# Performance work log

Measured on AMD Instinct MI355X. Metric: run time of the kernel, lower is better.

The kernel has to match this reference:

```python
import jax, jax.numpy as jnp
import numpy as np

ALPHA = 100.0  # self.softmax_alpha


def _interp_nearest(x, size):
    # torch F.interpolate mode='nearest': src_idx = floor(dst_idx * H_in / H_out)
    H, W = x.shape[-2], x.shape[-1]
    h, w = size
    ri = (jnp.arange(h) * H) // h
    ci = (jnp.arange(w) * W) // w
    return x[:, :, ri, :][:, :, :, ci]


def _interp_bilinear_ac(x, size):
    # torch F.interpolate mode='bilinear', align_corners=True
    H, W = x.shape[-2], x.shape[-1]
    h, w = size

    def coords(n_out, n_in):
        if n_out == 1:
            return jnp.zeros((1,), jnp.float32)
        return jnp.arange(n_out, dtype=jnp.float32) * ((n_in - 1) / (n_out - 1))

    ry, rx = coords(h, H), coords(w, W)
    y0 = jnp.floor(ry).astype(jnp.int32)
    x0 = jnp.floor(rx).astype(jnp.int32)
    y1 = jnp.clip(y0 + 1, 0, H - 1)
    x1 = jnp.clip(x0 + 1, 0, W - 1)
    wy = (ry - y0.astype(jnp.float32))[None, None, :, None]
    wx = (rx - x0.astype(jnp.float32))[None, None, None, :]
    rows = x[:, :, y0, :] * (1.0 - wy) + x[:, :, y1, :] * wy  # (n,c,h,W)
    return rows[:, :, :, x0] * (1.0 - wx) + rows[:, :, :, x1] * wx  # (n,c,h,w)


def _warp(unalign_fb, fa, fa_parse, fb, fb_parse, alpha):
    n, c, h, w = fa.shape
    c2 = unalign_fb.shape[1]
    hw = h * w
    # center and channel-normalize features per spatial location
    fa = fa - jnp.mean(fa, axis=(2, 3), keepdims=True)
    fb = fb - jnp.mean(fb, axis=(2, 3), keepdims=True)
    fa = fa.reshape(n, c, hw)
    fb = fb.reshape(n, c, hw)
    fa = fa / jnp.linalg.norm(fa, axis=1, keepdims=True)
    fb = fb / jnp.linalg.norm(fb, axis=1, keepdims=True)
    ufb = unalign_fb.reshape(n, c2, hw)
    mask_a = (fa_parse.reshape(n, -1, hw)[:, 1:, :] != 0).astype(fa.dtype)  # (n,K,hw)
    mask_b = (fb_parse.reshape(n, -1, hw)[:, 1:, :] != 0).astype(fb.dtype)
    local_fa = fa[:, None, :, :] * mask_a[:, :, None, :]  # (n,K,c,hw)
    local_fb = fb[:, None, :, :] * mask_b[:, :, None, :]  # (n,K,c,hw)
    # energy[n,k,q,p] = sum_c local_fb[n,k,c,q] * local_fa[n,k,c,p]
    energy = jnp.einsum('nkcq,nkcp->nkqp', local_fb, local_fa) * alpha
    corr = jax.nn.softmax(energy, axis=2)  # softmax over fb locations q
    warped = jnp.einsum('ncq,nkqp->nkcp', ufb, corr)  # (n,K,c2,hw)
    combined = (warped * mask_a[:, :, None, :]).sum(axis=1)  # (n,c2,hw)
    norm = jnp.maximum(mask_a.sum(axis=1, keepdims=True), 1.0)  # (n,1,hw)
    aligned = combined / norm
    return aligned.reshape(n, c2, h, w)


def setup_inputs() -> dict:
    key = jax.random.key(0)
    k1, k2, k3, k4, k5 = jax.random.split(key, 5)
    return {
        'unalign_fb': jax.random.normal(k1, (1, 64, 256, 256), jnp.float32),
        'fa': jax.random.normal(k2, (1, 256, 64, 64), jnp.float32),
        'fa_parse': jax.random.randint(k3, (1, 4, 256, 256), 0, 2).astype(jnp.int32),
        'fb': jax.random.normal(k4, (1, 256, 64, 64), jnp.float32),
        'fb_parse': jax.random.randint(k5, (1, 4, 256, 256), 0, 2).astype(jnp.int32),
    }


def reference(unalign_fb, fa, fa_parse, fb, fb_parse):
    raw_hw = unalign_fb.shape[-2:]
    feat_hw = fa.shape[-2:]
    fa_p = _interp_nearest(fa_parse, feat_hw)
    fb_p = _interp_nearest(fb_parse, feat_hw)
    ufb = _interp_bilinear_ac(unalign_fb, fb.shape[-2:])
    aligned = _warp(ufb, fa, fa_p, fb, fb_p, ALPHA)
    return _interp_bilinear_ac(aligned, raw_hw)
```

## Files before the change

### kernel.cpp

```cpp
#include <hip/hip_runtime.h>
#include <math.h>

#define HW 4096
#define CC 256
#define C2 64
#define E50f 1.928749848e-22f

typedef unsigned short USH;
typedef __attribute__((ext_vector_type(8))) _Float16 f16x8;
typedef __attribute__((ext_vector_type(8))) short bf8;
typedef __attribute__((ext_vector_type(4))) float f32x4;

__device__ __forceinline__ USH f2bf(float x) {
    unsigned u = __float_as_uint(x);
    u += 0x7fff + ((u >> 16) & 1);
    return (USH)(u >> 16);
}
__device__ __forceinline__ USH f2h(float x) {
    _Float16 h = (_Float16)x;
    return *(USH*)&h;
}

__device__ __forceinline__ void gl2lds16(const USH* g, USH* l) {
    __builtin_amdgcn_global_load_lds(
        (const __attribute__((address_space(1))) void*)g,
        (__attribute__((address_space(3))) void*)l, 16, 0, 0);
}

__global__ void k_prep1(const float* __restrict__ fa, const float* __restrict__ fb,
                        float* __restrict__ mu,
                        const float* __restrict__ ufb_src, const int* __restrict__ fb_parse,
                        USH* __restrict__ vtT, float* __restrict__ bgp) {
    __shared__ float4 sred[256];
    int t = threadIdx.x;
    if (blockIdx.x < 512) {
        int b = blockIdx.x;
        const float* src = (b < CC) ? (fa + b * HW) : (fb + (b - CC) * HW);
        float s = 0.f;
        for (int q = t; q < HW; q += 256) s += src[q];
        sred[t].x = s;
        __syncthreads();
        for (int st = 128; st > 0; st >>= 1) {
            if (t < st) sred[t].x += sred[t + st].x;
            __syncthreads();
        }
        if (t == 0) mu[b] = sred[0].x * (1.0f / HW);
        return;
    }
    int bid = blockIdx.x - 512;
    int pblk = bid & 15, c = bid >> 4;
    int p = pblk * 256 + t;
    int j = p >> 6, i = p & 63;
    int off = (4 * j) * 256 + 4 * i;
    float m0 = (fb_parse[1 * 65536 + off] != 0) ? 1.f : 0.f;
    float m1 = (fb_parse[2 * 65536 + off] != 0) ? 1.f : 0.f;
    float m2 = (fb_parse[3 * 65536 + off] != 0) ? 1.f : 0.f;
    float ry = j * (255.0f / 63.0f);
    int y0 = (int)ry; y0 = min(y0, 255); int y1 = min(y0 + 1, 255);
    float wy = ry - (float)y0;
    float rx = i * (255.0f / 63.0f);
    int x0 = (int)rx; x0 = min(x0, 255); int x1 = min(x0 + 1, 255);
    float wx = rx - (float)x0;
    const float* sc = ufb_src + c * 65536;
    float r0 = sc[y0 * 256 + x0] * (1.f - wx) + sc[y0 * 256 + x1] * wx;
    float r1 = sc[y1 * 256 + x0] * (1.f - wx) + sc[y1 * 256 + x1] * wx;
    float v = r0 * (1.f - wy) + r1 * wy;
    size_t cbase = (size_t)(p >> 5) * 8192 + (p & 31);
    vtT[cbase + (0 * 65 + c) * 32] = f2bf(v * m0);
    vtT[cbase + (1 * 65 + c) * 32] = f2bf(v * m1);
    vtT[cbase + (2 * 65 + c) * 32] = f2bf(v * m2);
    if (c == 0) {
        vtT[cbase + 64 * 32]  = f2bf(m0);
        vtT[cbase + 129 * 32] = f2bf(m1);
        vtT[cbase + 194 * 32] = f2bf(m2);
        for (int m = 195; m < 256; ++m) vtT[cbase + m * 32] = 0;
    }
    sred[t] = make_float4(v, v * m0, v * m1, v * m2);
    __syncthreads();
    for (int st = 128; st > 0; st >>= 1) {
        if (t < st) {
            float4 o = sred[t + st];
            sred[t].x += o.x; sred[t].y += o.y; sred[t].z += o.z; sred[t].w += o.w;
        }
        __syncthreads();
    }
    if (t == 0) {
        float4 r = sred[0];
        bgp[pblk * 320 + 256 + c]     = r.x;
        bgp[pblk * 320 + 0 * 65 + c]  = r.y;
        bgp[pblk * 320 + 1 * 65 + c]  = r.z;
        bgp[pblk * 320 + 2 * 65 + c]  = r.w;
    }
    __syncthreads();
    if (c == 0) {
        sred[t] = make_float4(m0, m1, m2, 0.f);
        __syncthreads();
        for (int st = 128; st > 0; st >>= 1) {
            if (t < st) {
                float4 o = sred[t + st];
                sred[t].x += o.x; sred[t].y += o.y; sred[t].z += o.z;
            }
            __syncthreads();
        }
        if (t == 0) {
            float4 r = sred[0];
            bgp[pblk * 320 + 64]  = r.x;
            bgp[pblk * 320 + 129] = r.y;
            bgp[pblk * 320 + 194] = r.z;
        }
    }
}

__global__ void k_norm_ss(const float* __restrict__ fa, const float* __restrict__ fb,
                          const float* __restrict__ mu, float* __restrict__ ssq_part) {
    int which = blockIdx.z;
    const float* src = which ? fb : fa;
    int p = blockIdx.x * 256 + threadIdx.x;
    int c0 = blockIdx.y * 32;
    float ss = 0.f;
    for (int c = c0; c < c0 + 32; ++c) {
        float v = src[c * HW + p] - mu[which * CC + c];
        ss += v * v;
    }
    ssq_part[(which * 8 + blockIdx.y) * HW + p] = ss;
}

__global__ __launch_bounds__(256) void k_norm_split_t(
    const float* __restrict__ fa, const float* __restrict__ fb,
    const float* __restrict__ mu, const float* __restrict__ ssq_part,
    USH* __restrict__ faT, USH* __restrict__ fbT) {
    __shared__ float tile[64][68];
    int which = blockIdx.z;
    const float* src = which ? fb : fa;
    USH* dst = which ? fbT : faT;
    int p0 = blockIdx.x * 64;
    int c0 = blockIdx.y * 64;
    int t = threadIdx.x;
    {
        int c_r = t >> 2, seg = t & 3;
        const float* s = &src[(size_t)(c0 + c_r) * HW + p0 + seg * 16];
#pragma unroll
        for (int k = 0; k < 4; ++k)
            *(float4*)&tile[c_r][seg * 16 + k * 4] = *(const float4*)&s[k * 4];
    }
    __syncthreads();
    {
        int p_r = t >> 2, seg = t & 3;
        int cl = seg * 16;
        float ss = 0.f;
#pragma unroll
        for (int z = 0; z < 8; ++z) ss += ssq_part[(which * 8 + z) * HW + p0 + p_r];
        float rinv = rsqrtf(ss);
        union { USH us[8]; uint4 v; } h0, h1;
#pragma unroll
        for (int j = 0; j < 8; ++j)
            h0.us[j] = f2h((tile[cl + j][p_r] - mu[which * CC + c0 + cl + j]) * rinv);
#pragma unroll
        for (int j = 0; j < 8; ++j)
            h1.us[j] = f2h((tile[cl + 8 + j][p_r] - mu[which * CC + c0 + cl + 8 + j]) * rinv);
        int kc = (c0 >> 5) + (seg >> 1);
        size_t base = (size_t)kc * 131072 + (size_t)(p0 + p_r) * 32 + (seg & 1) * 16;
        *(uint4*)&dst[base] = h0.v;
        *(uint4*)&dst[base + 8] = h1.v;
    }
}

__global__ __launch_bounds__(256, 2) void k_attn(
    const USH* __restrict__ faT, const USH* __restrict__ fbT,
    const USH* __restrict__ vtT, float* __restrict__ part) {
    __shared__ USH sA[2][2048];
    __shared__ USH sB[2][4096];
    __shared__ USH sV[2][8192];
    __shared__ USH sE[64 * 136];
    int t = threadIdx.x;
    int p0 = blockIdx.x * 64;
    int z = blockIdx.y;
    int w = t >> 6, lane = t & 63, lr = lane & 15, quad = lane >> 4;
    f32x4 accp[4][4] = {};

    const USH* gA = faT + (size_t)p0 * 32;

#define DMA_AB(buf, kc, q0)                                                          \
    do {                                                                             \
        gl2lds16(gA + (size_t)(kc) * 131072 + w * 512 + lane * 8, &sA[buf][w * 512]);\
        _Pragma("unroll")                                                            \
        for (int cc = 0; cc < 2; ++cc)                                               \
            gl2lds16(fbT + (size_t)(kc) * 131072 + (size_t)(q0) * 32 +               \
                         (2 * w + cc) * 512 + lane * 8,                              \
                     &sB[buf][(2 * w + cc) * 512]);                                  \
    } while (0)
#define DMA_V(buf, qc)                                                               \
    do {                                                                             \
        _Pragma("unroll")                                                            \
        for (int cc = 0; cc < 4; ++cc)                                               \
            gl2lds16(vtT + (size_t)(qc) * 8192 + (4 * w + cc) * 512 + lane * 8,      \
                     &sV[buf][(4 * w + cc) * 512]);                                  \
    } while (0)

    DMA_AB(0, 0, z * 512);
    __syncthreads();
    for (int qt = 0; qt < 4; ++qt) {
        int q0 = z * 512 + qt * 128;
        f32x4 accs[2][4] = {};
        for (int kc = 0; kc < 8; ++kc) {
            int cur = kc & 1;
            if (kc < 7) DMA_AB(cur ^ 1, kc + 1, q0);
            else        DMA_V(0, z * 16 + qt * 4);
            f16x8 a[2], b[4];
#pragma unroll
            for (int i = 0; i < 2; ++i)
                a[i] = *(const f16x8*)&sB[cur][(32 * w + 16 * i + lr) * 32 + quad * 8];
#pragma unroll
            for (int jj = 0; jj < 4; ++jj)
                b[jj] = *(const f16x8*)&sA[cur][(16 * jj + lr) * 32 + quad * 8];
#pragma unroll
            for (int i = 0; i < 2; ++i)
#pragma unroll
                for (int jj = 0; jj < 4; ++jj)
                    accs[i][jj] = __builtin_amdgcn_mfma_f32_16x16x32_f16(a[i], b[jj], accs[i][jj], 0, 0, 0);
            __syncthreads();
        }
#pragma unroll
        for (int i = 0; i < 2; ++i)
#pragma unroll
            for (int jj = 0; jj < 4; ++jj) {
                unsigned u0 = ((unsigned)f2bf(__expf(fmaf(100.f, accs[i][jj][1], -50.f))) << 16)
                            | (unsigned)f2bf(__expf(fmaf(100.f, accs[i][jj][0], -50.f)));
                unsigned u1 = ((unsigned)f2bf(__expf(fmaf(100.f, accs[i][jj][3], -50.f))) << 16)
                            | (unsigned)f2bf(__expf(fmaf(100.f, accs[i][jj][2], -50.f)));
                int addr = (16 * jj + lr) * 136 + 32 * w + 16 * i + 4 * quad;
                uint2 u; u.x = u0; u.y = u1;
                *(uint2*)&sE[addr] = u;
            }
        __syncthreads();
        for (int kc = 0; kc < 4; ++kc) {
            int cur = kc & 1;
            if (kc < 3)      DMA_V(cur ^ 1, z * 16 + qt * 4 + kc + 1);
            else if (qt < 3) DMA_AB(0, 0, q0 + 128);
            bf8 av[4], be[4];
#pragma unroll
            for (int i = 0; i < 4; ++i)
                av[i] = *(const bf8*)&sV[cur][(64 * w + 16 * i + lr) * 32 + quad * 8];
#pragma unroll
            for (int jj = 0; jj < 4; ++jj)
                be[jj] = *(const bf8*)&sE[(16 * jj + lr) * 136 + kc * 32 + quad * 8];
#pragma unroll
            for (int i = 0; i < 4; ++i)
#pragma unroll
                for (int jj = 0; jj < 4; ++jj)
                    accp[i][jj] = __builtin_amdgcn_mfma_f32_16x16x32_bf16(av[i], be[jj], accp[i][jj], 0, 0, 0);
            __syncthreads();
        }
    }
#undef DMA_AB
#undef DMA_V
    float* op = part + (size_t)z * 1048576;
#pragma unroll
    for (int i = 0; i < 4; ++i) {
        int m = 64 * w + 16 * i + quad * 4;
#pragma unroll
        for (int jj = 0; jj < 4; ++jj) {
            int pc = p0 + 16 * jj + lr;
#pragma unroll
            for (int r = 0; r < 4; ++r)
                op[(size_t)(m + r) * HW + pc] = accp[i][jj][r];
        }
    }
}

__global__ void k_combine8(const float* __restrict__ part, const float* __restrict__ bgp,
                           const int* __restrict__ fa_parse, float* __restrict__ aligned) {
    __shared__ float sums[8];
    int t = threadIdx.x;
    int c2 = blockIdx.y;
    if (t < 7) {
        int idx = (t < 3) ? (t * 65 + 64) : ((t < 6) ? (t - 3) * 65 + c2 : 256 + c2);
        float s = 0.f;
#pragma unroll
        for (int pb = 0; pb < 16; ++pb) s += bgp[pb * 320 + idx];
        sums[t] = s;
    }
    __syncthreads();
    int p = blockIdx.x * 256 + t;
    int jj = p >> 6, ii = p & 63;
    int off = (4 * jj) * 256 + 4 * ii;
    float num = 0.f, s = 0.f;
    for (int k = 0; k < 3; ++k) {
        float ma = (fa_parse[(k + 1) * 65536 + off] != 0) ? 1.f : 0.f;
        s += ma;
        float den = E50f * (4096.0f - sums[k]);
        float nu  = E50f * (sums[6] - sums[3 + k]);
        size_t rd = (size_t)(k * 65 + 64) * HW + p;
        size_t rn = (size_t)(k * 65 + c2) * HW + p;
#pragma unroll
        for (int z = 0; z < 8; ++z) {
            den += part[(size_t)z * 1048576 + rd];
            nu  += part[(size_t)z * 1048576 + rn];
        }
        num += ma * (nu / den);
    }
    aligned[c2 * HW + p] = num / fmaxf(s, 1.f);
}

__global__ void k_bilin_up(const float* __restrict__ aligned, float* __restrict__ out) {
    int idx = (blockIdx.x * 256 + threadIdx.x) * 4;
    int c2 = blockIdx.y;
    int y = idx >> 8;
    float ry = y * (63.0f / 255.0f);
    int y0 = (int)ry; y0 = min(y0, 63); int y1 = min(y0 + 1, 63);
    float wy = ry - (float)y0;
    const float* a = aligned + c2 * HW;
    float4 o;
    float* op = &o.x;
#pragma unroll
    for (int u = 0; u < 4; ++u) {
        int x = (idx & 255) + u;
        float rx = x * (63.0f / 255.0f);
        int x0 = (int)rx; x0 = min(x0, 63); int x1 = min(x0 + 1, 63);
        float wx = rx - (float)x0;
        float r0 = a[y0 * 64 + x0] * (1.f - wx) + a[y0 * 64 + x1] * wx;
        float r1 = a[y1 * 64 + x0] * (1.f - wx) + a[y1 * 64 + x1] * wx;
        op[u] = r0 * (1.f - wy) + r1 * wy;
    }
    *(float4*)&out[c2 * 65536 + idx] = o;
}

extern "C" void kernel_launch(void* const* d_in, const int* in_sizes, int n_in,
                              void* d_out, int out_size, void* d_ws, size_t ws_size,
                              hipStream_t stream) {
    const float* unalign_fb = (const float*)d_in[0];
    const float* fa         = (const float*)d_in[1];
    const int*   fa_parse   = (const int*)d_in[2];
    const float* fb         = (const float*)d_in[3];
    const int*   fb_parse   = (const int*)d_in[4];
    float* out = (float*)d_out;

    float* w = (float*)d_ws;
    float* mu       = w;
    float* ssq_part = w + 512;
    float* bgp      = w + 66048;
    float* part     = w + 71168;
    float* aligned  = w + 8459776;
    USH* faT = (USH*)(w + 8721920);
    USH* fbT = (USH*)(w + 9246208);
    USH* vtT = (USH*)(w + 9770496);

    k_prep1<<<dim3(1536), dim3(256), 0, stream>>>(fa, fb, mu, unalign_fb, fb_parse, vtT, bgp);
    k_norm_ss<<<dim3(16, 8, 2), dim3(256), 0, stream>>>(fa, fb, mu, ssq_part);
    k_norm_split_t<<<dim3(64, 4, 2), dim3(256), 0, stream>>>(fa, fb, mu, ssq_part, faT, fbT);
    k_attn<<<dim3(64, 8), dim3(256), 0, stream>>>(faT, fbT, vtT, part);
    k_combine8<<<dim3(16, 64), dim3(256), 0, stream>>>(part, bgp, fa_parse, aligned);
    k_bilin_up<<<dim3(64, 64), dim3(256), 0, stream>>>(aligned, out);
}
```

Baseline: 136.3 us.

## Fold mean-centering and normalization into attention epilogue via algebraic correction

The separate mean, sum-of-squares and normalize passes are replaced by a single prep pass that writes raw fp16 transposed features plus per-location squared sums and column sums. A tiny stats kernel and a correction kernel then compute per-location mean dot products and inverse norms, and the attention epilogue applies centering and scaling algebraically to the raw dot products before the exponential. Separately, the V tile is now read directly from global memory instead of being staged in LDS, which frees shared memory so the launch bound can allow 3 blocks. The risks are precision loss from subtracting large terms on uncentered fp16 data (amplified by alpha=100) and extra global-load latency in the PV loop.

```diff
diff --git a/kernel.cpp b/kernel.cpp
--- a/kernel.cpp
+++ b/kernel.cpp
@@ -20,6 +20,10 @@
     _Float16 h = (_Float16)x;
     return *(USH*)&h;
 }
+__device__ __forceinline__ float h2f(USH u) {
+    _Float16 h = *(_Float16*)&u;
+    return (float)h;
+}
 
 __device__ __forceinline__ void gl2lds16(const USH* g, USH* l) {
     __builtin_amdgcn_global_load_lds(
@@ -27,27 +31,74 @@
         (__attribute__((address_space(3))) void*)l, 16, 0, 0);
 }
 
-__global__ void k_prep1(const float* __restrict__ fa, const float* __restrict__ fb,
-                        float* __restrict__ mu,
-                        const float* __restrict__ ufb_src, const int* __restrict__ fb_parse,
-                        USH* __restrict__ vtT, float* __restrict__ bgp) {
+__global__ __launch_bounds__(256) void k_prep(
+    const float* __restrict__ fa, const float* __restrict__ fb,
+    USH* __restrict__ faT, USH* __restrict__ fbT,
+    float* __restrict__ Sxx, float* __restrict__ colsum,
+    const float* __restrict__ ufb_src, const int* __restrict__ fb_parse,
+    USH* __restrict__ vtT, float* __restrict__ bgp) {
+    __shared__ float tile[64][68];
+    __shared__ float cs[64][4];
+    __shared__ float sx[64][4];
     __shared__ float4 sred[256];
     int t = threadIdx.x;
-    if (blockIdx.x < 512) {
-        int b = blockIdx.x;
-        const float* src = (b < CC) ? (fa + b * HW) : (fb + (b - CC) * HW);
-        float s = 0.f;
-        for (int q = t; q < HW; q += 256) s += src[q];
-        sred[t].x = s;
-        __syncthreads();
-        for (int st = 128; st > 0; st >>= 1) {
-            if (t < st) sred[t].x += sred[t + st].x;
+    if (blockIdx.x < 128) {
+        int which = blockIdx.x & 1;
+        int pblk = blockIdx.x >> 1;
+        int p0 = pblk * 64;
+        const float* src = which ? fb : fa;
+        USH* dst = which ? fbT : faT;
+        int c_r = t >> 2, seg = t & 3;
+        float sxx_acc = 0.f;
+        for (int ci = 0; ci < 4; ++ci) {
+            int c0 = ci * 64;
+            float lsum = 0.f;
+            {
+                const float* s = &src[(size_t)(c0 + c_r) * HW + p0 + seg * 16];
+#pragma unroll
+                for (int k = 0; k < 4; ++k) {
+                    float4 v = *(const float4*)&s[k * 4];
+                    *(float4*)&tile[c_r][seg * 16 + k * 4] = v;
+                    lsum += v.x + v.y + v.z + v.w;
+                }
+            }
+            cs[c_r][seg] = lsum;
             __syncthreads();
-        }
-        if (t == 0) mu[b] = sred[0].x * (1.0f / HW);
+            if (t < 64)
+                colsum[(which * 64 + pblk) * 256 + c0 + t] =
+                    cs[t][0] + cs[t][1] + cs[t][2] + cs[t][3];
+            {
+                int p_r = c_r;
+                int cl = seg * 16;
+                union { USH us[8]; uint4 v; } h0, h1;
+#pragma unroll
+                for (int j = 0; j < 8; ++j) {
+                    USH h = f2h(tile[cl + j][p_r]);
+                    float xv = h2f(h);
+                    sxx_acc += xv * xv;
+                    h0.us[j] = h;
+                }
+#pragma unroll
+                for (int j = 0; j < 8; ++j) {
+                    USH h = f2h(tile[cl + 8 + j][p_r]);
+                    float xv = h2f(h);
+                    sxx_acc += xv * xv;
+                    h1.us[j] = h;
+                }
+                int kc = ci * 2 + (seg >> 1);
+                size_t base = (size_t)kc * 131072 + (size_t)(p0 + p_r) * 32 + (seg & 1) * 16;
+                *(uint4*)&dst[base] = h0.v;
+                *(uint4*)&dst[base + 8] = h1.v;
+            }
+            __syncthreads();
+        }
+        sx[c_r][seg] = sxx_acc;
+        __syncthreads();
+        if (t < 64)
+            Sxx[which * HW + p0 + t] = sx[t][0] + sx[t][1] + sx[t][2] + sx[t][3];
         return;
     }
-    int bid = blockIdx.x - 512;
+    int bid = blockIdx.x - 128;
     int pblk = bid & 15, c = bid >> 4;
     int p = pblk * 256 + t;
     int j = p >> 6, i = p & 63;
@@ -111,66 +162,76 @@
     }
 }
 
-__global__ void k_norm_ss(const float* __restrict__ fa, const float* __restrict__ fb,
-                          const float* __restrict__ mu, float* __restrict__ ssq_part) {
-    int which = blockIdx.z;
-    const float* src = which ? fb : fa;
-    int p = blockIdx.x * 256 + threadIdx.x;
-    int c0 = blockIdx.y * 32;
-    float ss = 0.f;
-    for (int c = c0; c < c0 + 32; ++c) {
-        float v = src[c * HW + p] - mu[which * CC + c];
-        ss += v * v;
-    }
-    ssq_part[(which * 8 + blockIdx.y) * HW + p] = ss;
-}
-
-__global__ __launch_bounds__(256) void k_norm_split_t(
-    const float* __restrict__ fa, const float* __restrict__ fb,
-    const float* __restrict__ mu, const float* __restrict__ ssq_part,
-    USH* __restrict__ faT, USH* __restrict__ fbT) {
-    __shared__ float tile[64][68];
-    int which = blockIdx.z;
-    const float* src = which ? fb : fa;
-    USH* dst = which ? fbT : faT;
-    int p0 = blockIdx.x * 64;
-    int c0 = blockIdx.y * 64;
+__global__ void k_stats(const float* __restrict__ colsum, float* __restrict__ stats) {
+    __shared__ float4 sred[256];
     int t = threadIdx.x;
-    {
-        int c_r = t >> 2, seg = t & 3;
-        const float* s = &src[(size_t)(c0 + c_r) * HW + p0 + seg * 16];
-#pragma unroll
-        for (int k = 0; k < 4; ++k)
-            *(float4*)&tile[c_r][seg * 16 + k * 4] = *(const float4*)&s[k * 4];
-    }
-    __syncthreads();
-    {
-        int p_r = t >> 2, seg = t & 3;
-        int cl = seg * 16;
-        float ss = 0.f;
-#pragma unroll
-        for (int z = 0; z < 8; ++z) ss += ssq_part[(which * 8 + z) * HW + p0 + p_r];
-        float rinv = rsqrtf(ss);
-        union { USH us[8]; uint4 v; } h0, h1;
-#pragma unroll
-        for (int j = 0; j < 8; ++j)
-            h0.us[j] = f2h((tile[cl + j][p_r] - mu[which * CC + c0 + cl + j]) * rinv);
-#pragma unroll
-        for (int j = 0; j < 8; ++j)
-            h1.us[j] = f2h((tile[cl + 8 + j][p_r] - mu[which * CC + c0 + cl + 8 + j]) * rinv);
-        int kc = (c0 >> 5) + (seg >> 1);
-        size_t base = (size_t)kc * 131072 + (size_t)(p0 + p_r) * 32 + (seg & 1) * 16;
-        *(uint4*)&dst[base] = h0.v;
-        *(uint4*)&dst[base + 8] = h1.v;
-    }
-}
-
-__global__ __launch_bounds__(256, 2) void k_attn(
+    float s0 = 0.f, s1 = 0.f;
+    for (int pb = 0; pb < 64; ++pb) {
+        s0 += colsum[(0 * 64 + pb) * 256 + t];
+        s1 += colsum[(1 * 64 + pb) * 256 + t];
+    }
+    float mu0 = s0 * (1.0f / HW), mu1 = s1 * (1.0f / HW);
+    stats[t] = mu0;
+    stats[256 + t] = mu1;
+    sred[t] = make_float4(mu0 * mu1, mu0 * mu0, mu1 * mu1, 0.f);
+    __syncthreads();
+    for (int st = 128; st > 0; st >>= 1) {
+        if (t < st) {
+            float4 o = sred[t + st];
+            sred[t].x += o.x; sred[t].y += o.y; sred[t].z += o.z;
+        }
+        __syncthreads();
+    }
+    if (t == 0) {
+        stats[512] = sred[0].x;
+        stats[513] = sred[0].y;
+        stats[514] = sred[0].z;
+    }
+}
+
+__global__ void k_corr(const USH* __restrict__ faT, const USH* __restrict__ fbT,
+                       const float* __restrict__ Sxx, const float* __restrict__ stats,
+                       float* __restrict__ dra) {
+    __shared__ float smu[512];
+    __shared__ float scc[4];
+    int t = threadIdx.x;
+    int which = blockIdx.y;
+    smu[t] = stats[t];
+    smu[256 + t] = stats[256 + t];
+    if (t < 3) scc[t] = stats[512 + t];
+    __syncthreads();
+    int p = blockIdx.x * 256 + t;
+    const USH* xT = which ? fbT : faT;
+    const float* mu_self = &smu[which * 256];
+    const float* mu_oth  = &smu[(1 - which) * 256];
+    float ca = 0.f, da = 0.f;
+    for (int kc = 0; kc < 8; ++kc) {
+        union { uint4 v; USH us[8]; } u[4];
+        size_t base = (size_t)kc * 131072 + (size_t)p * 32;
+#pragma unroll
+        for (int g = 0; g < 4; ++g) u[g].v = *(const uint4*)&xT[base + g * 8];
+#pragma unroll
+        for (int g = 0; g < 4; ++g)
+#pragma unroll
+            for (int jj = 0; jj < 8; ++jj) {
+                float xv = h2f(u[g].us[jj]);
+                int c = kc * 32 + g * 8 + jj;
+                ca += xv * mu_self[c];
+                da += xv * mu_oth[c];
+            }
+    }
+    float Sself = scc[1 + which];
+    float ra = rsqrtf(Sxx[which * HW + p] - 2.f * ca + Sself);
+    dra[which * HW + p] = da;
+    dra[2 * HW + which * HW + p] = ra;
+}
+
+__global__ __launch_bounds__(256, 3) void k_attn(
     const USH* __restrict__ faT, const USH* __restrict__ fbT,
-    const USH* __restrict__ vtT, float* __restrict__ part) {
+    const USH* __restrict__ vtT, const float* __restrict__ dra,
+    const float* __restrict__ stats, float* __restrict__ part) {
     __shared__ USH sA[2][2048];
     __shared__ USH sB[2][4096];
-    __shared__ USH sV[2][8192];
     __shared__ USH sE[64 * 136];
     int t = threadIdx.x;
     int p0 = blockIdx.x * 64;
@@ -179,6 +240,13 @@
     f32x4 accp[4][4] = {};
 
     const USH* gA = faT + (size_t)p0 * 32;
+    float Kc = stats[512];
+    float da4[4], ra4[4];
+#pragma unroll
+    for (int jj = 0; jj < 4; ++jj) {
+        da4[jj] = dra[p0 + 16 * jj + lr];
+        ra4[jj] = dra[2 * HW + p0 + 16 * jj + lr];
+    }
 
 #define DMA_AB(buf, kc, q0)                                                          \
     do {                                                                             \
@@ -189,13 +257,6 @@
                          (2 * w + cc) * 512 + lane * 8,                              \
                      &sB[buf][(2 * w + cc) * 512]);                                  \
     } while (0)
-#define DMA_V(buf, qc)                                                               \
-    do {                                                                             \
-        _Pragma("unroll")                                                            \
-        for (int cc = 0; cc < 4; ++cc)                                               \
-            gl2lds16(vtT + (size_t)(qc) * 8192 + (4 * w + cc) * 512 + lane * 8,      \
-                     &sV[buf][(4 * w + cc) * 512]);                                  \
-    } while (0)
 
     DMA_AB(0, 0, z * 512);
     __syncthreads();
@@ -204,8 +265,8 @@
         f32x4 accs[2][4] = {};
         for (int kc = 0; kc < 8; ++kc) {
             int cur = kc & 1;
-            if (kc < 7) DMA_AB(cur ^ 1, kc + 1, q0);
-            else        DMA_V(0, z * 16 + qt * 4);
+            if (kc < 7)      DMA_AB(cur ^ 1, kc + 1, q0);
+            else if (qt < 3) DMA_AB(0, 0, q0 + 128);
             f16x8 a[2], b[4];
 #pragma unroll
             for (int i = 0; i < 2; ++i)
@@ -221,26 +282,35 @@
             __syncthreads();
         }
 #pragma unroll
-        for (int i = 0; i < 2; ++i)
+        for (int i = 0; i < 2; ++i) {
+            int qb = q0 + 32 * w + 16 * i + 4 * quad;
+            float4 db4 = *(const float4*)&dra[HW + qb];
+            float4 rb4 = *(const float4*)&dra[3 * HW + qb];
 #pragma unroll
             for (int jj = 0; jj < 4; ++jj) {
-                unsigned u0 = ((unsigned)f2bf(__expf(fmaf(100.f, accs[i][jj][1], -50.f))) << 16)
-                            | (unsigned)f2bf(__expf(fmaf(100.f, accs[i][jj][0], -50.f)));
-                unsigned u1 = ((unsigned)f2bf(__expf(fmaf(100.f, accs[i][jj][3], -50.f))) << 16)
-                            | (unsigned)f2bf(__expf(fmaf(100.f, accs[i][jj][2], -50.f)));
+                float rr = ra4[jj];
+                float dd = da4[jj] - Kc;
+                float s0 = (accs[i][jj][0] - dd - db4.x) * (rr * rb4.x);
+                float s1 = (accs[i][jj][1] - dd - db4.y) * (rr * rb4.y);
+                float s2 = (accs[i][jj][2] - dd - db4.z) * (rr * rb4.z);
+                float s3 = (accs[i][jj][3] - dd - db4.w) * (rr * rb4.w);
+                unsigned u0 = ((unsigned)f2bf(__expf(fmaf(100.f, s1, -50.f))) << 16)
+                            | (unsigned)f2bf(__expf(fmaf(100.f, s0, -50.f)));
+                unsigned u1 = ((unsigned)f2bf(__expf(fmaf(100.f, s3, -50.f))) << 16)
+                            | (unsigned)f2bf(__expf(fmaf(100.f, s2, -50.f)));
                 int addr = (16 * jj + lr) * 136 + 32 * w + 16 * i + 4 * quad;
                 uint2 u; u.x = u0; u.y = u1;
                 *(uint2*)&sE[addr] = u;
             }
-        __syncthreads();
+        }
+        __syncthreads();
+#pragma unroll
         for (int kc = 0; kc < 4; ++kc) {
-            int cur = kc & 1;
-            if (kc < 3)      DMA_V(cur ^ 1, z * 16 + qt * 4 + kc + 1);
-            else if (qt < 3) DMA_AB(0, 0, q0 + 128);
+            size_t vbase = (size_t)(z * 16 + qt * 4 + kc) * 8192 + (size_t)quad * 8;
             bf8 av[4], be[4];
 #pragma unroll
             for (int i = 0; i < 4; ++i)
-                av[i] = *(const bf8*)&sV[cur][(64 * w + 16 * i + lr) * 32 + quad * 8];
+                av[i] = *(const bf8*)&vtT[vbase + (64 * w + 16 * i + lr) * 32];
 #pragma unroll
             for (int jj = 0; jj < 4; ++jj)
                 be[jj] = *(const bf8*)&sE[(16 * jj + lr) * 136 + kc * 32 + quad * 8];
@@ -249,11 +319,10 @@
 #pragma unroll
                 for (int jj = 0; jj < 4; ++jj)
                     accp[i][jj] = __builtin_amdgcn_mfma_f32_16x16x32_bf16(av[i], be[jj], accp[i][jj], 0, 0, 0);
-            __syncthreads();
-        }
+        }
+        __syncthreads();
     }
 #undef DMA_AB
-#undef DMA_V
     float* op = part + (size_t)z * 1048576;
 #pragma unroll
     for (int i = 0; i < 4; ++i) {
@@ -336,19 +405,22 @@
     float* out = (float*)d_out;
 
     float* w = (float*)d_ws;
-    float* mu       = w;
-    float* ssq_part = w + 512;
-    float* bgp      = w + 66048;
-    float* part     = w + 71168;
-    float* aligned  = w + 8459776;
-    USH* faT = (USH*)(w + 8721920);
-    USH* fbT = (USH*)(w + 9246208);
-    USH* vtT = (USH*)(w + 9770496);
-
-    k_prep1<<<dim3(1536), dim3(256), 0, stream>>>(fa, fb, mu, unalign_fb, fb_parse, vtT, bgp);
-    k_norm_ss<<<dim3(16, 8, 2), dim3(256), 0, stream>>>(fa, fb, mu, ssq_part);
-    k_norm_split_t<<<dim3(64, 4, 2), dim3(256), 0, stream>>>(fa, fb, mu, ssq_part, faT, fbT);
-    k_attn<<<dim3(64, 8), dim3(256), 0, stream>>>(faT, fbT, vtT, part);
+    float* stats   = w;
+    float* colsum  = w + 1024;
+    float* Sxx     = w + 33792;
+    float* dra     = w + 41984;
+    float* bgp     = w + 58368;
+    float* part    = w + 63488;
+    float* aligned = w + 8452096;
+    USH* faT = (USH*)(w + 8714240);
+    USH* fbT = (USH*)(w + 9238528);
+    USH* vtT = (USH*)(w + 9762816);
+
+    k_prep<<<dim3(1152), dim3(256), 0, stream>>>(fa, fb, faT, fbT, Sxx, colsum,
+                                                 unalign_fb, fb_parse, vtT, bgp);
+    k_stats<<<dim3(1), dim3(256), 0, stream>>>(colsum, stats);
+    k_corr<<<dim3(16, 2), dim3(256), 0, stream>>>(faT, fbT, Sxx, stats, dra);
+    k_attn<<<dim3(64, 8), dim3(256), 0, stream>>>(faT, fbT, vtT, dra, stats, part);
     k_combine8<<<dim3(16, 64), dim3(256), 0, stream>>>(part, bgp, fa_parse, aligned);
     k_bilin_up<<<dim3(64, 64), dim3(256), 0, stream>>>(aligned, out);
 }
```

After: 146.7 us. 1.08x slower.
